# Kernel tuning notes

Hardware: AMD Instinct MI355X
Metric: run time of the kernel (lower is better)

Reference implementation:

```python
import jax, jax.numpy as jnp
import numpy as np

N_SRC = 131072
N_DST = 65536
N_EDGES = 524288
D_IN = 128
D_OUT = 128


def setup_inputs() -> dict:
    key = jax.random.key(0)
    k1, k2, k3, k4, k5 = jax.random.split(key, 5)
    feat = jax.random.normal(k1, (N_SRC, D_IN), dtype=jnp.float32)
    # xavier_uniform-ish scale for the two projections
    lim = float(np.sqrt(6.0 / (D_IN + D_OUT))) * np.sqrt(2.0)
    W_self = jax.random.uniform(k2, (D_IN, D_OUT), jnp.float32, -lim, lim)
    W_neigh = jax.random.uniform(k3, (D_IN, D_OUT), jnp.float32, -lim, lim)
    b_self = jnp.zeros((D_OUT,), jnp.float32)
    b_neigh = jnp.zeros((D_OUT,), jnp.float32)
    src_idx = jax.random.randint(k4, (N_EDGES,), 0, N_SRC, dtype=jnp.int32)
    dst_idx = jnp.sort(jax.random.randint(k5, (N_EDGES,), 0, N_DST, dtype=jnp.int32))
    return {
        "feat": feat,
        "W_self": W_self,
        "b_self": b_self,
        "W_neigh": W_neigh,
        "b_neigh": b_neigh,
        "src_idx": src_idx,
        "dst_idx": dst_idx,
        "num_row": N_DST,
    }


def reference(feat, W_self, b_self, W_neigh, b_neigh, src_idx, dst_idx, num_row):
    # h_self: destination-node features (first num_row rows)
    h_self = feat[:num_row, :]                              # [num_row, D_IN]
    # csrmm: mean aggregation of source neighbor features per destination row
    gathered = feat[src_idx]                                # [E, D_IN]
    neigh_sum = jax.ops.segment_sum(gathered, dst_idx, num_segments=num_row)
    deg = jax.ops.segment_sum(jnp.ones_like(dst_idx, dtype=feat.dtype), dst_idx,
                              num_segments=num_row)
    h_neigh = neigh_sum / jnp.maximum(deg, 1.0)[:, None]    # [num_row, D_IN]
    # dual linear projections
    rst = (h_self @ W_self + b_self) + (h_neigh @ W_neigh + b_neigh)
    return rst
```

## Files before the change

### kernel.cpp

```cpp
#include <hip/hip_runtime.h>
#include <hip/hip_bf16.h>

#define N_SRC   131072
#define N_DST   65536
#define D       128

typedef __bf16 bf16x8 __attribute__((ext_vector_type(8)));
typedef float  f32x4  __attribute__((ext_vector_type(4)));

#define CONV_BLOCKS 8192
#define W_BLOCKS    64

__global__ __launch_bounds__(256) void prep_kernel(
    const float* __restrict__ feat,
    const int*   __restrict__ dst, int n_edges, int n_bnd_blocks,
    const float* __restrict__ W_self, const float* __restrict__ W_neigh,
    __bf16* __restrict__ feat_bf,
    int*    __restrict__ row_start,
    __bf16* __restrict__ Wt_self, __bf16* __restrict__ Wt_neigh)
{
    const int b = blockIdx.x;
    const int t = threadIdx.x;

    if (b < CONV_BLOCKS) {
        const size_t i0 = ((size_t)b * 256 + t) * 8;
        const float4 a0 = *(const float4*)&feat[i0];
        const float4 a1 = *(const float4*)&feat[i0 + 4];
        bf16x8 o;
        o[0] = (__bf16)a0.x; o[1] = (__bf16)a0.y; o[2] = (__bf16)a0.z; o[3] = (__bf16)a0.w;
        o[4] = (__bf16)a1.x; o[5] = (__bf16)a1.y; o[6] = (__bf16)a1.z; o[7] = (__bf16)a1.w;
        *(bf16x8*)&feat_bf[i0] = o;
    } else if (b < CONV_BLOCKS + n_bnd_blocks) {
        const int e = (b - CONV_BLOCKS) * 256 + t;
        if (e < n_edges) {
            const int d    = dst[e];
            const int prev = (e == 0) ? -1 : dst[e - 1];
            for (int r = prev + 1; r <= d; ++r) row_start[r] = e;
            if (e == n_edges - 1)
                for (int r = d + 1; r <= N_DST; ++r) row_start[r] = n_edges;
        }
    } else {
        const int wb  = b - CONV_BLOCKS - n_bnd_blocks;
        const int idx = wb * 256 + t;
        const int k = idx >> 7, n = idx & 127;
        Wt_self [n * D + k] = (__bf16)W_self [k * D + n];
        Wt_neigh[n * D + k] = (__bf16)W_neigh[k * D + n];
    }
}

__global__ __launch_bounds__(256) void neigh_kernel(
    const __bf16* __restrict__ feat_bf,
    const int*    __restrict__ src,
    const int*    __restrict__ row_start,
    __bf16*       __restrict__ h_neigh)
{
    const int g    = threadIdx.x >> 4;
    const int lane = threadIdx.x & 15;
    const int row  = blockIdx.x * 16 + g;
    const int s0   = row_start[row];
    const int s1   = row_start[row + 1];
    const int co   = lane * 8;

    float acc[8] = {0.f, 0.f, 0.f, 0.f, 0.f, 0.f, 0.f, 0.f};

    for (int base = s0; base < s1; base += 8) {
        int idx[8];
        #pragma unroll
        for (int j = 0; j < 8; ++j) {
            const int e = base + j;
            idx[j] = src[e < s1 ? e : s1 - 1];
        }
        bf16x8 v[8];
        #pragma unroll
        for (int j = 0; j < 8; ++j)
            v[j] = *(const bf16x8*)&feat_bf[(size_t)idx[j] * D + co];
        #pragma unroll
        for (int j = 0; j < 8; ++j) {
            const float m = (base + j < s1) ? 1.0f : 0.0f;
            #pragma unroll
            for (int c = 0; c < 8; ++c)
                acc[c] = fmaf(m, (float)v[j][c], acc[c]);
        }
    }

    const float inv = 1.0f / fmaxf((float)(s1 - s0), 1.0f);
    bf16x8 o;
    #pragma unroll
    for (int c = 0; c < 8; ++c) o[c] = (__bf16)(acc[c] * inv);
    *(bf16x8*)&h_neigh[(size_t)row * D + co] = o;
}

#define MREP 2

__global__ __launch_bounds__(256) void gemm_kernel(
    const __bf16* __restrict__ feat_bf,
    const __bf16* __restrict__ h_neigh,
    const __bf16* __restrict__ Wt_self,
    const __bf16* __restrict__ Wt_neigh,
    const float*  __restrict__ b_self,
    const float*  __restrict__ b_neigh,
    float*        __restrict__ out)
{
    const int t    = threadIdx.x;
    const int w    = t >> 6;
    const int l    = t & 63;
    const int m16  = l & 15;
    const int quad = l >> 4;
    const int kb   = quad * 8;
    const int rowbase = blockIdx.x * (64 * MREP) + w * (16 * MREP);

    f32x4 acc[MREP][8];
    #pragma unroll
    for (int rp = 0; rp < MREP; ++rp)
        #pragma unroll
        for (int nb = 0; nb < 8; ++nb)
            acc[rp][nb] = (f32x4){0.f, 0.f, 0.f, 0.f};

    const __bf16* __restrict__ Aptr[2] = {feat_bf, h_neigh};
    const __bf16* __restrict__ Wptr[2] = {Wt_self, Wt_neigh};

    #pragma unroll
    for (int p = 0; p < 2; ++p) {
        const __bf16* __restrict__ A = Aptr[p];
        const __bf16* __restrict__ W = Wptr[p];
        #pragma unroll
        for (int ks = 0; ks < 4; ++ks) {
            bf16x8 afrag[MREP];
            #pragma unroll
            for (int rp = 0; rp < MREP; ++rp)
                afrag[rp] = *(const bf16x8*)&A[(size_t)(rowbase + rp * 16 + m16) * D + ks * 32 + kb];
            #pragma unroll
            for (int nb = 0; nb < 8; ++nb) {
                const bf16x8 bfrag = *(const bf16x8*)&W[(size_t)(nb * 16 + m16) * D + ks * 32 + kb];
                #pragma unroll
                for (int rp = 0; rp < MREP; ++rp)
                    acc[rp][nb] = __builtin_amdgcn_mfma_f32_16x16x32_bf16(
                        afrag[rp], bfrag, acc[rp][nb], 0, 0, 0);
            }
        }
    }

    #pragma unroll
    for (int nb = 0; nb < 8; ++nb) {
        const int col  = nb * 16 + m16;
        const float bias = b_self[col] + b_neigh[col];
        #pragma unroll
        for (int rp = 0; rp < MREP; ++rp) {
            const int orow0 = rowbase + rp * 16 + quad * 4;
            #pragma unroll
            for (int r = 0; r < 4; ++r)
                out[(size_t)(orow0 + r) * D + col] = acc[rp][nb][r] + bias;
        }
    }
}

extern "C" void kernel_launch(void* const* d_in, const int* in_sizes, int n_in,
                              void* d_out, int out_size, void* d_ws, size_t ws_size,
                              hipStream_t stream)
{
    const float* feat    = (const float*)d_in[0];
    const float* W_self  = (const float*)d_in[1];
    const float* b_self  = (const float*)d_in[2];
    const float* W_neigh = (const float*)d_in[3];
    const float* b_neigh = (const float*)d_in[4];
    const int*   src_idx = (const int*)d_in[5];
    const int*   dst_idx = (const int*)d_in[6];
    const int n_edges = in_sizes[5];

    char* ws = (char*)d_ws;
    __bf16* feat_bf  = (__bf16*)ws;
    __bf16* h_neigh  = feat_bf + (size_t)N_SRC * D;
    int*    row_start = (int*)(h_neigh + (size_t)N_DST * D);
    __bf16* Wt_self  = (__bf16*)(row_start + N_DST + 16);
    __bf16* Wt_neigh = Wt_self + D * D;

    const int n_bnd = (n_edges + 255) / 256;
    prep_kernel<<<CONV_BLOCKS + n_bnd + W_BLOCKS, 256, 0, stream>>>(
        feat, dst_idx, n_edges, n_bnd, W_self, W_neigh,
        feat_bf, row_start, Wt_self, Wt_neigh);

    neigh_kernel<<<N_DST / 16, 256, 0, stream>>>(feat_bf, src_idx, row_start, h_neigh);

    gemm_kernel<<<N_DST / (64 * MREP), 256, 0, stream>>>(
        feat_bf, h_neigh, Wt_self, Wt_neigh, b_self, b_neigh, (float*)d_out);
}
```

Measured before the change: 165.3 us.

## Fuse neighbor aggregation into GEMM kernel, aggregating directly into MFMA fragments

After: 175.4 us. 1.06x slower.

```diff
diff --git a/kernel.cpp b/kernel.cpp
--- a/kernel.cpp
+++ b/kernel.cpp
@@ -48,53 +48,10 @@
     }
 }
 
-__global__ __launch_bounds__(256) void neigh_kernel(
+__global__ __launch_bounds__(256) void fused_kernel(
     const __bf16* __restrict__ feat_bf,
     const int*    __restrict__ src,
     const int*    __restrict__ row_start,
-    __bf16*       __restrict__ h_neigh)
-{
-    const int g    = threadIdx.x >> 4;
-    const int lane = threadIdx.x & 15;
-    const int row  = blockIdx.x * 16 + g;
-    const int s0   = row_start[row];
-    const int s1   = row_start[row + 1];
-    const int co   = lane * 8;
-
-    float acc[8] = {0.f, 0.f, 0.f, 0.f, 0.f, 0.f, 0.f, 0.f};
-
-    for (int base = s0; base < s1; base += 8) {
-        int idx[8];
-        #pragma unroll
-        for (int j = 0; j < 8; ++j) {
-            const int e = base + j;
-            idx[j] = src[e < s1 ? e : s1 - 1];
-        }
-        bf16x8 v[8];
-        #pragma unroll
-        for (int j = 0; j < 8; ++j)
-            v[j] = *(const bf16x8*)&feat_bf[(size_t)idx[j] * D + co];
-        #pragma unroll
-        for (int j = 0; j < 8; ++j) {
-            const float m = (base + j < s1) ? 1.0f : 0.0f;
-            #pragma unroll
-            for (int c = 0; c < 8; ++c)
-                acc[c] = fmaf(m, (float)v[j][c], acc[c]);
-        }
-    }
-
-    const float inv = 1.0f / fmaxf((float)(s1 - s0), 1.0f);
-    bf16x8 o;
-    #pragma unroll
-    for (int c = 0; c < 8; ++c) o[c] = (__bf16)(acc[c] * inv);
-    *(bf16x8*)&h_neigh[(size_t)row * D + co] = o;
-}
-
-#define MREP 2
-
-__global__ __launch_bounds__(256) void gemm_kernel(
-    const __bf16* __restrict__ feat_bf,
-    const __bf16* __restrict__ h_neigh,
     const __bf16* __restrict__ Wt_self,
     const __bf16* __restrict__ Wt_neigh,
     const float*  __restrict__ b_self,
@@ -107,36 +64,77 @@
     const int m16  = l & 15;
     const int quad = l >> 4;
     const int kb   = quad * 8;
-    const int rowbase = blockIdx.x * (64 * MREP) + w * (16 * MREP);
+    const int rowbase = blockIdx.x * 64 + w * 16;
+    const int row  = rowbase + m16;
 
-    f32x4 acc[MREP][8];
+    const int s0 = row_start[row];
+    const int s1 = row_start[row + 1];
+
+    float accg[4][8];
     #pragma unroll
-    for (int rp = 0; rp < MREP; ++rp)
+    for (int ks = 0; ks < 4; ++ks)
         #pragma unroll
-        for (int nb = 0; nb < 8; ++nb)
-            acc[rp][nb] = (f32x4){0.f, 0.f, 0.f, 0.f};
+        for (int j = 0; j < 8; ++j) accg[ks][j] = 0.f;
 
-    const __bf16* __restrict__ Aptr[2] = {feat_bf, h_neigh};
-    const __bf16* __restrict__ Wptr[2] = {Wt_self, Wt_neigh};
+    for (int e = s0; e < s1; e += 4) {
+        const int e1 = (e + 1 < s1) ? e + 1 : e;
+        const int e2 = (e + 2 < s1) ? e + 2 : e;
+        const int e3 = (e + 3 < s1) ? e + 3 : e;
+        const int i0 = src[e];
+        const int i1 = src[e1];
+        const int i2 = src[e2];
+        const int i3 = src[e3];
+        bf16x8 v0[4], v1[4], v2[4], v3[4];
+        #pragma unroll
+        for (int ks = 0; ks < 4; ++ks) {
+            const int off = ks * 32 + kb;
+            v0[ks] = *(const bf16x8*)&feat_bf[(size_t)i0 * D + off];
+            v1[ks] = *(const bf16x8*)&feat_bf[(size_t)i1 * D + off];
+            v2[ks] = *(const bf16x8*)&feat_bf[(size_t)i2 * D + off];
+            v3[ks] = *(const bf16x8*)&feat_bf[(size_t)i3 * D + off];
+        }
+        const float m1 = (e + 1 < s1) ? 1.f : 0.f;
+        const float m2 = (e + 2 < s1) ? 1.f : 0.f;
+        const float m3 = (e + 3 < s1) ? 1.f : 0.f;
+        #pragma unroll
+        for (int ks = 0; ks < 4; ++ks)
+            #pragma unroll
+            for (int j = 0; j < 8; ++j) {
+                float a = accg[ks][j] + (float)v0[ks][j];
+                a = fmaf(m1, (float)v1[ks][j], a);
+                a = fmaf(m2, (float)v2[ks][j], a);
+                a = fmaf(m3, (float)v3[ks][j], a);
+                accg[ks][j] = a;
+            }
+    }
+
+    const float inv = 1.0f / fmaxf((float)(s1 - s0), 1.0f);
+    bf16x8 afragN[4];
+    #pragma unroll
+    for (int ks = 0; ks < 4; ++ks)
+        #pragma unroll
+        for (int j = 0; j < 8; ++j)
+            afragN[ks][j] = (__bf16)(accg[ks][j] * inv);
+
+    f32x4 acc[8];
+    #pragma unroll
+    for (int nb = 0; nb < 8; ++nb) acc[nb] = (f32x4){0.f, 0.f, 0.f, 0.f};
 
     #pragma unroll
-    for (int p = 0; p < 2; ++p) {
-        const __bf16* __restrict__ A = Aptr[p];
-        const __bf16* __restrict__ W = Wptr[p];
+    for (int ks = 0; ks < 4; ++ks) {
+        const bf16x8 aS = *(const bf16x8*)&feat_bf[(size_t)row * D + ks * 32 + kb];
         #pragma unroll
-        for (int ks = 0; ks < 4; ++ks) {
-            bf16x8 afrag[MREP];
-            #pragma unroll
-            for (int rp = 0; rp < MREP; ++rp)
-                afrag[rp] = *(const bf16x8*)&A[(size_t)(rowbase + rp * 16 + m16) * D + ks * 32 + kb];
-            #pragma unroll
-            for (int nb = 0; nb < 8; ++nb) {
-                const bf16x8 bfrag = *(const bf16x8*)&W[(size_t)(nb * 16 + m16) * D + ks * 32 + kb];
-                #pragma unroll
-                for (int rp = 0; rp < MREP; ++rp)
-                    acc[rp][nb] = __builtin_amdgcn_mfma_f32_16x16x32_bf16(
-                        afrag[rp], bfrag, acc[rp][nb], 0, 0, 0);
-            }
+        for (int nb = 0; nb < 8; ++nb) {
+            const bf16x8 bS = *(const bf16x8*)&Wt_self[(size_t)(nb * 16 + m16) * D + ks * 32 + kb];
+            acc[nb] = __builtin_amdgcn_mfma_f32_16x16x32_bf16(aS, bS, acc[nb], 0, 0, 0);
+        }
+    }
+    #pragma unroll
+    for (int ks = 0; ks < 4; ++ks) {
+        #pragma unroll
+        for (int nb = 0; nb < 8; ++nb) {
+            const bf16x8 bN = *(const bf16x8*)&Wt_neigh[(size_t)(nb * 16 + m16) * D + ks * 32 + kb];
+            acc[nb] = __builtin_amdgcn_mfma_f32_16x16x32_bf16(afragN[ks], bN, acc[nb], 0, 0, 0);
         }
     }
 
@@ -144,13 +142,10 @@
     for (int nb = 0; nb < 8; ++nb) {
         const int col  = nb * 16 + m16;
         const float bias = b_self[col] + b_neigh[col];
+        const int orow0 = rowbase + quad * 4;
         #pragma unroll
-        for (int rp = 0; rp < MREP; ++rp) {
-            const int orow0 = rowbase + rp * 16 + quad * 4;
-            #pragma unroll
-            for (int r = 0; r < 4; ++r)
-                out[(size_t)(orow0 + r) * D + col] = acc[rp][nb][r] + bias;
-        }
+        for (int r = 0; r < 4; ++r)
+            out[(size_t)(orow0 + r) * D + col] = acc[nb][r] + bias;
     }
 }
 
@@ -168,19 +163,17 @@
     const int n_edges = in_sizes[5];
 
     char* ws = (char*)d_ws;
-    __bf16* feat_bf  = (__bf16*)ws;
-    __bf16* h_neigh  = feat_bf + (size_t)N_SRC * D;
-    int*    row_start = (int*)(h_neigh + (size_t)N_DST * D);
-    __bf16* Wt_self  = (__bf16*)(row_start + N_DST + 16);
-    __bf16* Wt_neigh = Wt_self + D * D;
+    __bf16* feat_bf   = (__bf16*)ws;
+    int*    row_start = (int*)(feat_bf + (size_t)N_SRC * D);
+    __bf16* Wt_self   = (__bf16*)(row_start + N_DST + 16);
+    __bf16* Wt_neigh  = Wt_self + D * D;
 
     const int n_bnd = (n_edges + 255) / 256;
     prep_kernel<<<CONV_BLOCKS + n_bnd + W_BLOCKS, 256, 0, stream>>>(
         feat, dst_idx, n_edges, n_bnd, W_self, W_neigh,
         feat_bf, row_start, Wt_self, Wt_neigh);
 
-    neigh_kernel<<<N_DST / 16, 256, 0, stream>>>(feat_bf, src_idx, row_start, h_neigh);
-
-    gemm_kernel<<<N_DST / (64 * MREP), 256, 0, stream>>>(
-        feat_bf, h_neigh, Wt_self, Wt_neigh, b_self, b_neigh, (float*)d_out);
+    fused_kernel<<<N_DST / 64, 256, 0, stream>>>(
+        feat_bf, src_idx, row_start, Wt_self, Wt_neigh, b_self, b_neigh,
+        (float*)d_out);
 }
```

## Fuse neighbor aggregation and dual projection GEMM into one kernel via LDS

Applied to the files above, without the earlier changes.

After: 174.0 us. 1.05x slower.

```diff
diff --git a/kernel.cpp b/kernel.cpp
--- a/kernel.cpp
+++ b/kernel.cpp
@@ -10,6 +10,8 @@
 
 #define CONV_BLOCKS 8192
 #define W_BLOCKS    64
+
+#define HPITCH 136
 
 __global__ __launch_bounds__(256) void prep_kernel(
     const float* __restrict__ feat,
@@ -48,109 +50,99 @@
     }
 }
 
-__global__ __launch_bounds__(256) void neigh_kernel(
+__global__ __launch_bounds__(256) void fused_kernel(
     const __bf16* __restrict__ feat_bf,
     const int*    __restrict__ src,
     const int*    __restrict__ row_start,
-    __bf16*       __restrict__ h_neigh)
-{
-    const int g    = threadIdx.x >> 4;
-    const int lane = threadIdx.x & 15;
-    const int row  = blockIdx.x * 16 + g;
-    const int s0   = row_start[row];
-    const int s1   = row_start[row + 1];
-    const int co   = lane * 8;
-
-    float acc[8] = {0.f, 0.f, 0.f, 0.f, 0.f, 0.f, 0.f, 0.f};
-
-    for (int base = s0; base < s1; base += 8) {
-        int idx[8];
-        #pragma unroll
-        for (int j = 0; j < 8; ++j) {
-            const int e = base + j;
-            idx[j] = src[e < s1 ? e : s1 - 1];
-        }
-        bf16x8 v[8];
-        #pragma unroll
-        for (int j = 0; j < 8; ++j)
-            v[j] = *(const bf16x8*)&feat_bf[(size_t)idx[j] * D + co];
-        #pragma unroll
-        for (int j = 0; j < 8; ++j) {
-            const float m = (base + j < s1) ? 1.0f : 0.0f;
-            #pragma unroll
-            for (int c = 0; c < 8; ++c)
-                acc[c] = fmaf(m, (float)v[j][c], acc[c]);
-        }
-    }
-
-    const float inv = 1.0f / fmaxf((float)(s1 - s0), 1.0f);
-    bf16x8 o;
-    #pragma unroll
-    for (int c = 0; c < 8; ++c) o[c] = (__bf16)(acc[c] * inv);
-    *(bf16x8*)&h_neigh[(size_t)row * D + co] = o;
-}
-
-#define MREP 2
-
-__global__ __launch_bounds__(256) void gemm_kernel(
-    const __bf16* __restrict__ feat_bf,
-    const __bf16* __restrict__ h_neigh,
     const __bf16* __restrict__ Wt_self,
     const __bf16* __restrict__ Wt_neigh,
     const float*  __restrict__ b_self,
     const float*  __restrict__ b_neigh,
     float*        __restrict__ out)
 {
-    const int t    = threadIdx.x;
+    __shared__ __bf16 hs[16 * HPITCH];
+
+    const int t       = threadIdx.x;
+    const int rowbase = blockIdx.x * 16;
+
+    {
+        const int g    = t >> 4;
+        const int lane = t & 15;
+        const int row  = rowbase + g;
+        const int s0   = row_start[row];
+        const int s1   = row_start[row + 1];
+        const int co   = lane * 8;
+
+        float acc[8] = {0.f, 0.f, 0.f, 0.f, 0.f, 0.f, 0.f, 0.f};
+
+        for (int base = s0; base < s1; base += 8) {
+            int idx[8];
+            #pragma unroll
+            for (int j = 0; j < 8; ++j) {
+                const int e = base + j;
+                idx[j] = src[e < s1 ? e : s1 - 1];
+            }
+            bf16x8 v[8];
+            #pragma unroll
+            for (int j = 0; j < 8; ++j)
+                v[j] = *(const bf16x8*)&feat_bf[(size_t)idx[j] * D + co];
+            #pragma unroll
+            for (int j = 0; j < 8; ++j) {
+                const float m = (base + j < s1) ? 1.0f : 0.0f;
+                #pragma unroll
+                for (int c = 0; c < 8; ++c)
+                    acc[c] = fmaf(m, (float)v[j][c], acc[c]);
+            }
+        }
+
+        const float inv = 1.0f / fmaxf((float)(s1 - s0), 1.0f);
+        bf16x8 o;
+        #pragma unroll
+        for (int c = 0; c < 8; ++c) o[c] = (__bf16)(acc[c] * inv);
+        *(bf16x8*)&hs[g * HPITCH + co] = o;
+    }
+    __syncthreads();
+
     const int w    = t >> 6;
     const int l    = t & 63;
     const int m16  = l & 15;
     const int quad = l >> 4;
     const int kb   = quad * 8;
-    const int rowbase = blockIdx.x * (64 * MREP) + w * (16 * MREP);
 
-    f32x4 acc[MREP][8];
+    bf16x8 aN[4], aS[4];
     #pragma unroll
-    for (int rp = 0; rp < MREP; ++rp)
-        #pragma unroll
-        for (int nb = 0; nb < 8; ++nb)
-            acc[rp][nb] = (f32x4){0.f, 0.f, 0.f, 0.f};
+    for (int ks = 0; ks < 4; ++ks) {
+        aN[ks] = *(const bf16x8*)&hs[m16 * HPITCH + ks * 32 + kb];
+        aS[ks] = *(const bf16x8*)&feat_bf[(size_t)(rowbase + m16) * D + ks * 32 + kb];
+    }
 
-    const __bf16* __restrict__ Aptr[2] = {feat_bf, h_neigh};
-    const __bf16* __restrict__ Wptr[2] = {Wt_self, Wt_neigh};
-
+    f32x4 acc[2];
     #pragma unroll
-    for (int p = 0; p < 2; ++p) {
-        const __bf16* __restrict__ A = Aptr[p];
-        const __bf16* __restrict__ W = Wptr[p];
+    for (int nbl = 0; nbl < 2; ++nbl) {
+        const int nb = w * 2 + nbl;
+        f32x4 a = (f32x4){0.f, 0.f, 0.f, 0.f};
         #pragma unroll
         for (int ks = 0; ks < 4; ++ks) {
-            bf16x8 afrag[MREP];
-            #pragma unroll
-            for (int rp = 0; rp < MREP; ++rp)
-                afrag[rp] = *(const bf16x8*)&A[(size_t)(rowbase + rp * 16 + m16) * D + ks * 32 + kb];
-            #pragma unroll
-            for (int nb = 0; nb < 8; ++nb) {
-                const bf16x8 bfrag = *(const bf16x8*)&W[(size_t)(nb * 16 + m16) * D + ks * 32 + kb];
-                #pragma unroll
-                for (int rp = 0; rp < MREP; ++rp)
-                    acc[rp][nb] = __builtin_amdgcn_mfma_f32_16x16x32_bf16(
-                        afrag[rp], bfrag, acc[rp][nb], 0, 0, 0);
-            }
+            const bf16x8 bS = *(const bf16x8*)&Wt_self [(size_t)(nb * 16 + m16) * D + ks * 32 + kb];
+            a = __builtin_amdgcn_mfma_f32_16x16x32_bf16(aS[ks], bS, a, 0, 0, 0);
         }
+        #pragma unroll
+        for (int ks = 0; ks < 4; ++ks) {
+            const bf16x8 bN = *(const bf16x8*)&Wt_neigh[(size_t)(nb * 16 + m16) * D + ks * 32 + kb];
+            a = __builtin_amdgcn_mfma_f32_16x16x32_bf16(aN[ks], bN, a, 0, 0, 0);
+        }
+        acc[nbl] = a;
     }
 
     #pragma unroll
-    for (int nb = 0; nb < 8; ++nb) {
+    for (int nbl = 0; nbl < 2; ++nbl) {
+        const int nb   = w * 2 + nbl;
         const int col  = nb * 16 + m16;
         const float bias = b_self[col] + b_neigh[col];
+        const int orow0 = rowbase + quad * 4;
         #pragma unroll
-        for (int rp = 0; rp < MREP; ++rp) {
-            const int orow0 = rowbase + rp * 16 + quad * 4;
-            #pragma unroll
-            for (int r = 0; r < 4; ++r)
-                out[(size_t)(orow0 + r) * D + col] = acc[rp][nb][r] + bias;
-        }
+        for (int r = 0; r < 4; ++r)
+            out[(size_t)(orow0 + r) * D + col] = acc[nbl][r] + bias;
     }
 }
 
@@ -168,19 +160,17 @@
     const int n_edges = in_sizes[5];
 
     char* ws = (char*)d_ws;
-    __bf16* feat_bf  = (__bf16*)ws;
-    __bf16* h_neigh  = feat_bf + (size_t)N_SRC * D;
-    int*    row_start = (int*)(h_neigh + (size_t)N_DST * D);
-    __bf16* Wt_self  = (__bf16*)(row_start + N_DST + 16);
-    __bf16* Wt_neigh = Wt_self + D * D;
+    __bf16* feat_bf   = (__bf16*)ws;
+    int*    row_start = (int*)(feat_bf + (size_t)N_SRC * D);
+    __bf16* Wt_self   = (__bf16*)(row_start + N_DST + 16);
+    __bf16* Wt_neigh  = Wt_self + D * D;
 
     const int n_bnd = (n_edges + 255) / 256;
     prep_kernel<<<CONV_BLOCKS + n_bnd + W_BLOCKS, 256, 0, stream>>>(
         feat, dst_idx, n_edges, n_bnd, W_self, W_neigh,
         feat_bf, row_start, Wt_self, Wt_neigh);
 
-    neigh_kernel<<<N_DST / 16, 256, 0, stream>>>(feat_bf, src_idx, row_start, h_neigh);
-
-    gemm_kernel<<<N_DST / (64 * MREP), 256, 0, stream>>>(
-        feat_bf, h_neigh, Wt_self, Wt_neigh, b_self, b_neigh, (float*)d_out);
+    fused_kernel<<<N_DST / 16, 256, 0, stream>>>(
+        feat_bf, src_idx, row_start, Wt_self, Wt_neigh, b_self, b_neigh,
+        (float*)d_out);
 }
```

## Drop bf16 feature conversion pass; gather and GEMM read fp32 features directly

Applied to the files above, without the earlier changes.

New measurement: 170.4 us. +3.1%, slower.

```diff
diff --git a/kernel.cpp b/kernel.cpp
--- a/kernel.cpp
+++ b/kernel.cpp
@@ -8,30 +8,19 @@
 typedef __bf16 bf16x8 __attribute__((ext_vector_type(8)));
 typedef float  f32x4  __attribute__((ext_vector_type(4)));
 
-#define CONV_BLOCKS 8192
-#define W_BLOCKS    64
+#define W_BLOCKS 64
 
 __global__ __launch_bounds__(256) void prep_kernel(
-    const float* __restrict__ feat,
     const int*   __restrict__ dst, int n_edges, int n_bnd_blocks,
     const float* __restrict__ W_self, const float* __restrict__ W_neigh,
-    __bf16* __restrict__ feat_bf,
     int*    __restrict__ row_start,
     __bf16* __restrict__ Wt_self, __bf16* __restrict__ Wt_neigh)
 {
     const int b = blockIdx.x;
     const int t = threadIdx.x;
 
-    if (b < CONV_BLOCKS) {
-        const size_t i0 = ((size_t)b * 256 + t) * 8;
-        const float4 a0 = *(const float4*)&feat[i0];
-        const float4 a1 = *(const float4*)&feat[i0 + 4];
-        bf16x8 o;
-        o[0] = (__bf16)a0.x; o[1] = (__bf16)a0.y; o[2] = (__bf16)a0.z; o[3] = (__bf16)a0.w;
-        o[4] = (__bf16)a1.x; o[5] = (__bf16)a1.y; o[6] = (__bf16)a1.z; o[7] = (__bf16)a1.w;
-        *(bf16x8*)&feat_bf[i0] = o;
-    } else if (b < CONV_BLOCKS + n_bnd_blocks) {
-        const int e = (b - CONV_BLOCKS) * 256 + t;
+    if (b < n_bnd_blocks) {
+        const int e = b * 256 + t;
         if (e < n_edges) {
             const int d    = dst[e];
             const int prev = (e == 0) ? -1 : dst[e - 1];
@@ -40,7 +29,7 @@
                 for (int r = d + 1; r <= N_DST; ++r) row_start[r] = n_edges;
         }
     } else {
-        const int wb  = b - CONV_BLOCKS - n_bnd_blocks;
+        const int wb  = b - n_bnd_blocks;
         const int idx = wb * 256 + t;
         const int k = idx >> 7, n = idx & 127;
         Wt_self [n * D + k] = (__bf16)W_self [k * D + n];
@@ -49,10 +38,10 @@
 }
 
 __global__ __launch_bounds__(256) void neigh_kernel(
-    const __bf16* __restrict__ feat_bf,
-    const int*    __restrict__ src,
-    const int*    __restrict__ row_start,
-    __bf16*       __restrict__ h_neigh)
+    const float* __restrict__ feat,
+    const int*   __restrict__ src,
+    const int*   __restrict__ row_start,
+    __bf16*      __restrict__ h_neigh)
 {
     const int g    = threadIdx.x >> 4;
     const int lane = threadIdx.x & 15;
@@ -70,16 +59,24 @@
             const int e = base + j;
             idx[j] = src[e < s1 ? e : s1 - 1];
         }
-        bf16x8 v[8];
+        float4 va[8], vb[8];
         #pragma unroll
-        for (int j = 0; j < 8; ++j)
-            v[j] = *(const bf16x8*)&feat_bf[(size_t)idx[j] * D + co];
+        for (int j = 0; j < 8; ++j) {
+            const float* p = &feat[(size_t)idx[j] * D + co];
+            va[j] = *(const float4*)p;
+            vb[j] = *(const float4*)(p + 4);
+        }
         #pragma unroll
         for (int j = 0; j < 8; ++j) {
             const float m = (base + j < s1) ? 1.0f : 0.0f;
-            #pragma unroll
-            for (int c = 0; c < 8; ++c)
-                acc[c] = fmaf(m, (float)v[j][c], acc[c]);
+            acc[0] = fmaf(m, va[j].x, acc[0]);
+            acc[1] = fmaf(m, va[j].y, acc[1]);
+            acc[2] = fmaf(m, va[j].z, acc[2]);
+            acc[3] = fmaf(m, va[j].w, acc[3]);
+            acc[4] = fmaf(m, vb[j].x, acc[4]);
+            acc[5] = fmaf(m, vb[j].y, acc[5]);
+            acc[6] = fmaf(m, vb[j].z, acc[6]);
+            acc[7] = fmaf(m, vb[j].w, acc[7]);
         }
     }
 
@@ -93,7 +90,7 @@
 #define MREP 2
 
 __global__ __launch_bounds__(256) void gemm_kernel(
-    const __bf16* __restrict__ feat_bf,
+    const float*  __restrict__ feat,
     const __bf16* __restrict__ h_neigh,
     const __bf16* __restrict__ Wt_self,
     const __bf16* __restrict__ Wt_neigh,
@@ -116,27 +113,42 @@
         for (int nb = 0; nb < 8; ++nb)
             acc[rp][nb] = (f32x4){0.f, 0.f, 0.f, 0.f};
 
-    const __bf16* __restrict__ Aptr[2] = {feat_bf, h_neigh};
-    const __bf16* __restrict__ Wptr[2] = {Wt_self, Wt_neigh};
+    #pragma unroll
+    for (int ks = 0; ks < 4; ++ks) {
+        bf16x8 afrag[MREP];
+        #pragma unroll
+        for (int rp = 0; rp < MREP; ++rp) {
+            const float* ap = &feat[(size_t)(rowbase + rp * 16 + m16) * D + ks * 32 + kb];
+            const float4 a0 = *(const float4*)ap;
+            const float4 a1 = *(const float4*)(ap + 4);
+            afrag[rp][0] = (__bf16)a0.x; afrag[rp][1] = (__bf16)a0.y;
+            afrag[rp][2] = (__bf16)a0.z; afrag[rp][3] = (__bf16)a0.w;
+            afrag[rp][4] = (__bf16)a1.x; afrag[rp][5] = (__bf16)a1.y;
+            afrag[rp][6] = (__bf16)a1.z; afrag[rp][7] = (__bf16)a1.w;
+        }
+        #pragma unroll
+        for (int nb = 0; nb < 8; ++nb) {
+            const bf16x8 bfrag = *(const bf16x8*)&Wt_self[(size_t)(nb * 16 + m16) * D + ks * 32 + kb];
+            #pragma unroll
+            for (int rp = 0; rp < MREP; ++rp)
+                acc[rp][nb] = __builtin_amdgcn_mfma_f32_16x16x32_bf16(
+                    afrag[rp], bfrag, acc[rp][nb], 0, 0, 0);
+        }
+    }
 
     #pragma unroll
-    for (int p = 0; p < 2; ++p) {
-        const __bf16* __restrict__ A = Aptr[p];
-        const __bf16* __restrict__ W = Wptr[p];
+    for (int ks = 0; ks < 4; ++ks) {
+        bf16x8 afrag[MREP];
         #pragma unroll
-        for (int ks = 0; ks < 4; ++ks) {
-            bf16x8 afrag[MREP];
+        for (int rp = 0; rp < MREP; ++rp)
+            afrag[rp] = *(const bf16x8*)&h_neigh[(size_t)(rowbase + rp * 16 + m16) * D + ks * 32 + kb];
+        #pragma unroll
+        for (int nb = 0; nb < 8; ++nb) {
+            const bf16x8 bfrag = *(const bf16x8*)&Wt_neigh[(size_t)(nb * 16 + m16) * D + ks * 32 + kb];
             #pragma unroll
             for (int rp = 0; rp < MREP; ++rp)
-                afrag[rp] = *(const bf16x8*)&A[(size_t)(rowbase + rp * 16 + m16) * D + ks * 32 + kb];
-            #pragma unroll
-            for (int nb = 0; nb < 8; ++nb) {
-                const bf16x8 bfrag = *(const bf16x8*)&W[(size_t)(nb * 16 + m16) * D + ks * 32 + kb];
-                #pragma unroll
-                for (int rp = 0; rp < MREP; ++rp)
-                    acc[rp][nb] = __builtin_amdgcn_mfma_f32_16x16x32_bf16(
-                        afrag[rp], bfrag, acc[rp][nb], 0, 0, 0);
-            }
+                acc[rp][nb] = __builtin_amdgcn_mfma_f32_16x16x32_bf16(
+                    afrag[rp], bfrag, acc[rp][nb], 0, 0, 0);
         }
     }
 
@@ -168,19 +180,18 @@
     const int n_edges = in_sizes[5];
 
     char* ws = (char*)d_ws;
-    __bf16* feat_bf  = (__bf16*)ws;
-    __bf16* h_neigh  = feat_bf + (size_t)N_SRC * D;
+    __bf16* h_neigh   = (__bf16*)ws;
     int*    row_start = (int*)(h_neigh + (size_t)N_DST * D);
-    __bf16* Wt_self  = (__bf16*)(row_start + N_DST + 16);
-    __bf16* Wt_neigh = Wt_self + D * D;
+    __bf16* Wt_self   = (__bf16*)(row_start + N_DST + 16);
+    __bf16* Wt_neigh  = Wt_self + D * D;
 
     const int n_bnd = (n_edges + 255) / 256;
-    prep_kernel<<<CONV_BLOCKS + n_bnd + W_BLOCKS, 256, 0, stream>>>(
-        feat, dst_idx, n_edges, n_bnd, W_self, W_neigh,
-        feat_bf, row_start, Wt_self, Wt_neigh);
+    prep_kernel<<<n_bnd + W_BLOCKS, 256, 0, stream>>>(
+        dst_idx, n_edges, n_bnd, W_self, W_neigh,
+        row_start, Wt_self, Wt_neigh);
 
-    neigh_kernel<<<N_DST / 16, 256, 0, stream>>>(feat_bf, src_idx, row_start, h_neigh);
+    neigh_kernel<<<N_DST / 16, 256, 0, stream>>>(feat, src_idx, row_start, h_neigh);
 
     gemm_kernel<<<N_DST / (64 * MREP), 256, 0, stream>>>(
-        feat_bf, h_neigh, Wt_self, Wt_neigh, b_self, b_neigh, (float*)d_out);
+        feat, h_neigh, Wt_self, Wt_neigh, b_self, b_neigh, (float*)d_out);
 }
```
